# Kernel tuning notes

Measured on AMD Instinct MI355X. Metric: run time of the kernel, lower is better.

Reference implementation:

```python
import jax, jax.numpy as jnp
import numpy as np

B, N = 2048, 16384
K = 256
TEMPERATURE = 1.0


def entmax15(z):
    # alpha=1.5 entmax via exact sort-based threshold (Peters et al. 2019).
    z = z / 2.0
    zs = jnp.flip(jnp.sort(z, axis=-1), axis=-1)          # descending sort [B, N]
    rho = jnp.arange(1, z.shape[-1] + 1, dtype=z.dtype)   # 1..N
    mean = jnp.cumsum(zs, axis=-1) / rho
    mean_sq = jnp.cumsum(zs * zs, axis=-1) / rho
    ss = rho * (mean_sq - mean * mean)
    delta = jnp.clip((1.0 - ss) / rho, 0.0)
    tau = mean - jnp.sqrt(delta)                           # candidate thresholds
    support = jnp.sum(tau <= zs, axis=-1, keepdims=True)   # support size per row
    tau_star = jnp.take_along_axis(tau, support - 1, axis=-1)
    p = jnp.clip(z - tau_star, 0.0) ** 2
    return p


def setup_inputs() -> dict:
    key = jax.random.key(0)
    logits = jax.random.normal(key, (B, N), dtype=jnp.float32)
    return {"logits": logits}


def reference(logits):
    weights = entmax15(logits / TEMPERATURE)
    # top-k mask + renormalize
    _, topk_idx = jax.lax.top_k(weights, K)                # [B, K]
    mask = jnp.zeros_like(weights).at[
        jnp.arange(weights.shape[0])[:, None], topk_idx
    ].set(1.0)
    weights = weights * mask
    weights = weights / (jnp.sum(weights, axis=-1, keepdims=True) + 1e-8)
    num_selected = jnp.sum(weights > 1e-6, axis=-1)
    return weights, num_selected
```

## Files before the change

### kernel.cpp

```cpp
#include <hip/hip_runtime.h>
#include <math.h>

#define BROWS 2048
#define NCOLS 16384
#define NT    1024
#define V4PT  (NCOLS / NT / 4)
#define CAP   512

__global__ __launch_bounds__(NT, 8)
void entmax_fused(const float* __restrict__ in, float* __restrict__ outw,
                  float* __restrict__ outn)
{
    __shared__ float red[4][16];
    __shared__ float redm[16];
    __shared__ float cand[CAP + 4];
    __shared__ float s_zm, s_T, s_tau, s_S;
    __shared__ int   s_cnt, s_nsel;

    const int row  = blockIdx.x;
    const int tid  = threadIdx.x;
    const int lane = tid & 63;
    const int wid  = tid >> 6;
    const float4* rp4 = (const float4*)(in + (size_t)row * NCOLS);
    float4*       wp4 = (float4*)(outw + (size_t)row * NCOLS);

    if (tid == 0) { s_cnt = 0; s_nsel = 0; }

    float4 zr[V4PT];
    float m = -INFINITY;
    #pragma unroll
    for (int it = 0; it < V4PT; ++it) {
        float4 v = rp4[it * NT + tid];
        v.x *= 0.5f; v.y *= 0.5f; v.z *= 0.5f; v.w *= 0.5f;
        zr[it] = v;
        m = fmaxf(m, fmaxf(fmaxf(v.x, v.y), fmaxf(v.z, v.w)));
    }
    #pragma unroll
    for (int off = 1; off < 64; off <<= 1) m = fmaxf(m, __shfl_xor(m, off));
    if (lane == 0) redm[wid] = m;
    __syncthreads();
    if (tid < 64) {
        float v = (lane < 16) ? redm[lane] : -INFINITY;
        #pragma unroll
        for (int off = 1; off < 16; off <<= 1) v = fmaxf(v, __shfl_xor(v, off));
        if (lane == 0) s_zm = v;
    }
    __syncthreads();
    const float zm = s_zm;

    float g0 = 0.f, g1 = 0.f, g2 = 0.f, g3 = 0.f;
    #pragma unroll
    for (int it = 0; it < V4PT; ++it) {
        float4 v = zr[it];
        #pragma unroll
        for (int e = 0; e < 4; ++e) {
            float z = (e == 0) ? v.x : (e == 1) ? v.y : (e == 2) ? v.z : v.w;
            float d3 = z - (zm - 1.0f);
            if (d3 > 0.f) {
                g3 = fmaf(d3, d3, g3);
                float d2 = d3 - 0.25f; if (d2 > 0.f) g2 = fmaf(d2, d2, g2);
                float d1 = d3 - 0.50f; if (d1 > 0.f) g1 = fmaf(d1, d1, g1);
                float d0 = d3 - 0.75f; if (d0 > 0.f) g0 = fmaf(d0, d0, g0);
            }
        }
    }
    #pragma unroll
    for (int off = 1; off < 64; off <<= 1) {
        g0 += __shfl_xor(g0, off); g1 += __shfl_xor(g1, off);
        g2 += __shfl_xor(g2, off); g3 += __shfl_xor(g3, off);
    }
    if (lane == 0) { red[0][wid] = g0; red[1][wid] = g1; red[2][wid] = g2; red[3][wid] = g3; }
    __syncthreads();
    if (tid < 64) {
        int j = lane >> 4, idx = lane & 15;
        float v = red[j][idx];
        #pragma unroll
        for (int off = 1; off < 16; off <<= 1) v += __shfl_xor(v, off);
        float G0 = __shfl(v, 0), G1 = __shfl(v, 16), G2 = __shfl(v, 32), G3 = __shfl(v, 48);
        (void)G3;
        if (lane == 0) {
            float T = zm - 1.0f;
            if      (G0 >= 1.02f) T = zm - 0.25f;
            else if (G1 >= 1.02f) T = zm - 0.50f;
            else if (G2 >= 1.02f) T = zm - 0.75f;
            s_T = T;
        }
    }
    __syncthreads();
    const float T = s_T;

    #pragma unroll
    for (int it = 0; it < V4PT; ++it) {
        float4 v = zr[it];
        if (v.x > T) { int p = atomicAdd(&s_cnt, 1); if (p < CAP) cand[p] = v.x; }
        if (v.y > T) { int p = atomicAdd(&s_cnt, 1); if (p < CAP) cand[p] = v.y; }
        if (v.z > T) { int p = atomicAdd(&s_cnt, 1); if (p < CAP) cand[p] = v.z; }
        if (v.w > T) { int p = atomicAdd(&s_cnt, 1); if (p < CAP) cand[p] = v.w; }
    }
    __syncthreads();

    if (tid < 64) {
        const int C = min(s_cnt, CAP);
        if (lane < 4) cand[C + lane] = -INFINITY;
        const int C4 = (C + 3) >> 2;
        const float4* c4 = (const float4*)cand;
        float lo = T, hi = zm;
        for (int round = 0; round < 3; ++round) {
            float h = (hi - lo) * 0.015625f;
            float t = fmaf(h, (float)(lane + 1), lo);
            float g = 0.f;
            for (int i = 0; i < C4; ++i) {
                float4 v = c4[i]; float d;
                d = v.x - t; if (d > 0.f) g = fmaf(d, d, g);
                d = v.y - t; if (d > 0.f) g = fmaf(d, d, g);
                d = v.z - t; if (d > 0.f) g = fmaf(d, d, g);
                d = v.w - t; if (d > 0.f) g = fmaf(d, d, g);
            }
            unsigned long long bal = __ballot(g >= 1.f);
            float lo_old = lo;
            if (bal == 0ull) hi = lo_old + h;
            else {
                int j = 63 - (int)__clzll((long long)bal);
                lo = fmaf(h, (float)(j + 1), lo_old);
                hi = fmaf(h, (float)(j + 2), lo_old);
            }
        }
        float tau = lo;
        for (int r = 0; r < 3; ++r) {
            float k = 0.f, s1 = 0.f, s2 = 0.f;
            for (int i = 0; i < C4; ++i) {
                float4 v = c4[i];
                if (v.x > tau) { k += 1.f; s1 += v.x; s2 = fmaf(v.x, v.x, s2); }
                if (v.y > tau) { k += 1.f; s1 += v.y; s2 = fmaf(v.y, v.y, s2); }
                if (v.z > tau) { k += 1.f; s1 += v.z; s2 = fmaf(v.z, v.z, s2); }
                if (v.w > tau) { k += 1.f; s1 += v.w; s2 = fmaf(v.w, v.w, s2); }
            }
            if (k < 0.5f) break;
            float mean  = s1 / k;
            float ss    = s2 - mean * s1;
            float delta = fmaxf((1.f - ss) / k, 0.f);
            tau = mean - sqrtf(delta);
        }
        float ps = 0.f;
        for (int i = 0; i < C4; ++i) {
            float4 v = c4[i]; float d;
            d = v.x - tau; if (d > 0.f) ps = fmaf(d, d, ps);
            d = v.y - tau; if (d > 0.f) ps = fmaf(d, d, ps);
            d = v.z - tau; if (d > 0.f) ps = fmaf(d, d, ps);
            d = v.w - tau; if (d > 0.f) ps = fmaf(d, d, ps);
        }
        if (lane == 0) { s_tau = tau; s_S = ps; }
    }
    __syncthreads();
    const float tau_star = s_tau;
    const float rnorm    = 1.0f / (s_S + 1e-8f);

    int lc = 0;
    #pragma unroll
    for (int it = 0; it < V4PT; ++it) {
        float4 v = zr[it];
        float4 w; float d;
        d = fmaxf(v.x - tau_star, 0.f); w.x = d * d * rnorm; lc += (w.x > 1e-6f);
        d = fmaxf(v.y - tau_star, 0.f); w.y = d * d * rnorm; lc += (w.y > 1e-6f);
        d = fmaxf(v.z - tau_star, 0.f); w.z = d * d * rnorm; lc += (w.z > 1e-6f);
        d = fmaxf(v.w - tau_star, 0.f); w.w = d * d * rnorm; lc += (w.w > 1e-6f);
        wp4[it * NT + tid] = w;
    }
    #pragma unroll
    for (int off = 32; off; off >>= 1) lc += __shfl_down(lc, off);
    if (lane == 0) atomicAdd(&s_nsel, lc);
    __syncthreads();
    if (tid == 0) outn[row] = (float)s_nsel;
}

extern "C" void kernel_launch(void* const* d_in, const int* in_sizes, int n_in,
                              void* d_out, int out_size, void* d_ws, size_t ws_size,
                              hipStream_t stream) {
    const float* logits = (const float*)d_in[0];
    float* outw = (float*)d_out;
    float* outn = outw + (size_t)BROWS * NCOLS;
    entmax_fused<<<dim3(BROWS), dim3(NT), 0, stream>>>(logits, outw, outn);
}
```

Measured before the change: 254.0 us.

## Shrink blocks to 256 threads and re-read row from global instead of registers

Switches from a 1024-thread block that holds the whole row in registers to a 256-thread block that streams the row from global memory three times (max, histogram, output), relying on cache for the re-reads. Candidate collection moves into the histogram pass with a larger shared buffer, and a second compaction over that buffer replaces the separate full-row filter pass. Cross-wave reductions become simple serial sums over 4 waves. The aim is lower register pressure and higher occupancy, at the cost of extra global/L2 traffic and more shared-memory atomics on the wider candidate window.

New measurement: 264.6 us. 4.2% more time.

```diff
diff --git a/kernel.cpp b/kernel.cpp
--- a/kernel.cpp
+++ b/kernel.cpp
@@ -3,19 +3,21 @@
 
 #define BROWS 2048
 #define NCOLS 16384
-#define NT    1024
-#define V4PT  (NCOLS / NT / 4)
-#define CAP   512
+#define NT    256
+#define F4T   (NCOLS / NT / 4)
+#define LCAP  3072
+#define CCAP  512
 
 __global__ __launch_bounds__(NT, 8)
 void entmax_fused(const float* __restrict__ in, float* __restrict__ outw,
                   float* __restrict__ outn)
 {
-    __shared__ float red[4][16];
-    __shared__ float redm[16];
-    __shared__ float cand[CAP + 4];
+    __shared__ float cand[LCAP];
+    __shared__ float cand2[CCAP + 4];
+    __shared__ float red[4][4];
+    __shared__ float redm[4];
     __shared__ float s_zm, s_T, s_tau, s_S;
-    __shared__ int   s_cnt, s_nsel;
+    __shared__ int   s_cnt, s_cnt2, s_nsel;
 
     const int row  = blockIdx.x;
     const int tid  = threadIdx.x;
@@ -24,40 +26,35 @@
     const float4* rp4 = (const float4*)(in + (size_t)row * NCOLS);
     float4*       wp4 = (float4*)(outw + (size_t)row * NCOLS);
 
-    if (tid == 0) { s_cnt = 0; s_nsel = 0; }
+    if (tid == 0) { s_cnt = 0; s_cnt2 = 0; s_nsel = 0; }
 
-    float4 zr[V4PT];
     float m = -INFINITY;
-    #pragma unroll
-    for (int it = 0; it < V4PT; ++it) {
+    #pragma unroll 8
+    for (int it = 0; it < F4T; ++it) {
         float4 v = rp4[it * NT + tid];
-        v.x *= 0.5f; v.y *= 0.5f; v.z *= 0.5f; v.w *= 0.5f;
-        zr[it] = v;
         m = fmaxf(m, fmaxf(fmaxf(v.x, v.y), fmaxf(v.z, v.w)));
     }
     #pragma unroll
     for (int off = 1; off < 64; off <<= 1) m = fmaxf(m, __shfl_xor(m, off));
     if (lane == 0) redm[wid] = m;
     __syncthreads();
-    if (tid < 64) {
-        float v = (lane < 16) ? redm[lane] : -INFINITY;
-        #pragma unroll
-        for (int off = 1; off < 16; off <<= 1) v = fmaxf(v, __shfl_xor(v, off));
-        if (lane == 0) s_zm = v;
-    }
+    if (tid == 0)
+        s_zm = 0.5f * fmaxf(fmaxf(redm[0], redm[1]), fmaxf(redm[2], redm[3]));
     __syncthreads();
     const float zm = s_zm;
+    const float TL = zm - 1.0f;
 
     float g0 = 0.f, g1 = 0.f, g2 = 0.f, g3 = 0.f;
-    #pragma unroll
-    for (int it = 0; it < V4PT; ++it) {
-        float4 v = zr[it];
+    #pragma unroll 4
+    for (int it = 0; it < F4T; ++it) {
+        float4 v = rp4[it * NT + tid];
         #pragma unroll
         for (int e = 0; e < 4; ++e) {
-            float z = (e == 0) ? v.x : (e == 1) ? v.y : (e == 2) ? v.z : v.w;
-            float d3 = z - (zm - 1.0f);
+            float z  = 0.5f * ((e == 0) ? v.x : (e == 1) ? v.y : (e == 2) ? v.z : v.w);
+            float d3 = z - TL;
             if (d3 > 0.f) {
                 g3 = fmaf(d3, d3, g3);
+                int p = atomicAdd(&s_cnt, 1); if (p < LCAP) cand[p] = z;
                 float d2 = d3 - 0.25f; if (d2 > 0.f) g2 = fmaf(d2, d2, g2);
                 float d1 = d3 - 0.50f; if (d1 > 0.f) g1 = fmaf(d1, d1, g1);
                 float d0 = d3 - 0.75f; if (d0 > 0.f) g0 = fmaf(d0, d0, g0);
@@ -71,39 +68,33 @@
     }
     if (lane == 0) { red[0][wid] = g0; red[1][wid] = g1; red[2][wid] = g2; red[3][wid] = g3; }
     __syncthreads();
-    if (tid < 64) {
-        int j = lane >> 4, idx = lane & 15;
-        float v = red[j][idx];
-        #pragma unroll
-        for (int off = 1; off < 16; off <<= 1) v += __shfl_xor(v, off);
-        float G0 = __shfl(v, 0), G1 = __shfl(v, 16), G2 = __shfl(v, 32), G3 = __shfl(v, 48);
-        (void)G3;
-        if (lane == 0) {
-            float T = zm - 1.0f;
-            if      (G0 >= 1.02f) T = zm - 0.25f;
-            else if (G1 >= 1.02f) T = zm - 0.50f;
-            else if (G2 >= 1.02f) T = zm - 0.75f;
-            s_T = T;
-        }
+    if (tid == 0) {
+        float G0 = red[0][0] + red[0][1] + red[0][2] + red[0][3];
+        float G1 = red[1][0] + red[1][1] + red[1][2] + red[1][3];
+        float G2 = red[2][0] + red[2][1] + red[2][2] + red[2][3];
+        float T = TL;
+        if      (G0 >= 1.02f) T = zm - 0.25f;
+        else if (G1 >= 1.02f) T = zm - 0.50f;
+        else if (G2 >= 1.02f) T = zm - 0.75f;
+        s_T = T;
     }
     __syncthreads();
     const float T = s_T;
 
-    #pragma unroll
-    for (int it = 0; it < V4PT; ++it) {
-        float4 v = zr[it];
-        if (v.x > T) { int p = atomicAdd(&s_cnt, 1); if (p < CAP) cand[p] = v.x; }
-        if (v.y > T) { int p = atomicAdd(&s_cnt, 1); if (p < CAP) cand[p] = v.y; }
-        if (v.z > T) { int p = atomicAdd(&s_cnt, 1); if (p < CAP) cand[p] = v.z; }
-        if (v.w > T) { int p = atomicAdd(&s_cnt, 1); if (p < CAP) cand[p] = v.w; }
+    {
+        const int C = min(s_cnt, LCAP);
+        for (int i = tid; i < C; i += NT) {
+            float z = cand[i];
+            if (z > T) { int p = atomicAdd(&s_cnt2, 1); if (p < CCAP) cand2[p] = z; }
+        }
     }
     __syncthreads();
 
     if (tid < 64) {
-        const int C = min(s_cnt, CAP);
-        if (lane < 4) cand[C + lane] = -INFINITY;
+        const int C = min(s_cnt2, CCAP);
+        if (lane < 4) cand2[C + lane] = -INFINITY;
         const int C4 = (C + 3) >> 2;
-        const float4* c4 = (const float4*)cand;
+        const float4* c4 = (const float4*)cand2;
         float lo = T, hi = zm;
         for (int round = 0; round < 3; ++round) {
             float h = (hi - lo) * 0.015625f;
@@ -156,14 +147,14 @@
     const float rnorm    = 1.0f / (s_S + 1e-8f);
 
     int lc = 0;
-    #pragma unroll
-    for (int it = 0; it < V4PT; ++it) {
-        float4 v = zr[it];
+    #pragma unroll 8
+    for (int it = 0; it < F4T; ++it) {
+        float4 v = rp4[it * NT + tid];
         float4 w; float d;
-        d = fmaxf(v.x - tau_star, 0.f); w.x = d * d * rnorm; lc += (w.x > 1e-6f);
-        d = fmaxf(v.y - tau_star, 0.f); w.y = d * d * rnorm; lc += (w.y > 1e-6f);
-        d = fmaxf(v.z - tau_star, 0.f); w.z = d * d * rnorm; lc += (w.z > 1e-6f);
-        d = fmaxf(v.w - tau_star, 0.f); w.w = d * d * rnorm; lc += (w.w > 1e-6f);
+        d = fmaxf(0.5f * v.x - tau_star, 0.f); w.x = d * d * rnorm; lc += (w.x > 1e-6f);
+        d = fmaxf(0.5f * v.y - tau_star, 0.f); w.y = d * d * rnorm; lc += (w.y > 1e-6f);
+        d = fmaxf(0.5f * v.z - tau_star, 0.f); w.z = d * d * rnorm; lc += (w.z > 1e-6f);
+        d = fmaxf(0.5f * v.w - tau_star, 0.f); w.w = d * d * rnorm; lc += (w.w > 1e-6f);
         wp4[it * NT + tid] = w;
     }
     #pragma unroll
```

## Process two rows per block with wave-aggregated candidate compaction and nontemporal stores

Applied to the files above, without the earlier changes.

Each 1024-thread block now handles two rows at once. The two rows' reductions and threshold searches run interleaved, and two wavefronts work through the candidate lists in parallel, which is meant to hide the serial single-wave tail phase and the barrier latency. Candidate compaction now uses a ballot, popcount and one atomic per wave instead of a shared atomic per element, and the candidate cap is raised. Output stores use nontemporal hints. In exchange, register pressure doubles (32 float4 per thread), which risks spills or lower occupancy, and there are half as many blocks.

After: 266.6 us. 1.05x slower.

```diff
diff --git a/kernel.cpp b/kernel.cpp
--- a/kernel.cpp
+++ b/kernel.cpp
@@ -4,103 +4,176 @@
 #define BROWS 2048
 #define NCOLS 16384
 #define NT    1024
-#define V4PT  (NCOLS / NT / 4)
-#define CAP   512
+#define F4R   (NCOLS / NT / 4)
+#define CCAP  1024
+
+typedef float f32x4 __attribute__((ext_vector_type(4)));
 
 __global__ __launch_bounds__(NT, 8)
-void entmax_fused(const float* __restrict__ in, float* __restrict__ outw,
-                  float* __restrict__ outn)
+void entmax2(const float* __restrict__ in, float* __restrict__ outw,
+             float* __restrict__ outn)
 {
-    __shared__ float red[4][16];
-    __shared__ float redm[16];
-    __shared__ float cand[CAP + 4];
-    __shared__ float s_zm, s_T, s_tau, s_S;
-    __shared__ int   s_cnt, s_nsel;
-
-    const int row  = blockIdx.x;
+    __shared__ float candA[CCAP + 4], candB[CCAP + 4];
+    __shared__ float redA[4][16], redB[4][16];
+    __shared__ float redmA[16], redmB[16];
+    __shared__ float s_zmA, s_zmB, s_TA, s_TB, s_tauA, s_SA, s_tauB, s_SB;
+    __shared__ int   s_cntA, s_cntB, s_nselA, s_nselB;
+
+    const int pair = blockIdx.x;
+    const int rowA = pair * 2, rowB = pair * 2 + 1;
     const int tid  = threadIdx.x;
     const int lane = tid & 63;
     const int wid  = tid >> 6;
-    const float4* rp4 = (const float4*)(in + (size_t)row * NCOLS);
-    float4*       wp4 = (float4*)(outw + (size_t)row * NCOLS);
-
-    if (tid == 0) { s_cnt = 0; s_nsel = 0; }
-
-    float4 zr[V4PT];
-    float m = -INFINITY;
-    #pragma unroll
-    for (int it = 0; it < V4PT; ++it) {
-        float4 v = rp4[it * NT + tid];
-        v.x *= 0.5f; v.y *= 0.5f; v.z *= 0.5f; v.w *= 0.5f;
-        zr[it] = v;
-        m = fmaxf(m, fmaxf(fmaxf(v.x, v.y), fmaxf(v.z, v.w)));
-    }
-    #pragma unroll
-    for (int off = 1; off < 64; off <<= 1) m = fmaxf(m, __shfl_xor(m, off));
-    if (lane == 0) redm[wid] = m;
-    __syncthreads();
-    if (tid < 64) {
-        float v = (lane < 16) ? redm[lane] : -INFINITY;
+    const float4* rpA = (const float4*)(in + (size_t)rowA * NCOLS);
+    const float4* rpB = (const float4*)(in + (size_t)rowB * NCOLS);
+    f32x4*        wpA = (f32x4*)(outw + (size_t)rowA * NCOLS);
+    f32x4*        wpB = (f32x4*)(outw + (size_t)rowB * NCOLS);
+
+    if (tid == 0) { s_cntA = 0; s_cntB = 0; s_nselA = 0; s_nselB = 0; }
+
+    float4 zrA[F4R], zrB[F4R];
+    #pragma unroll
+    for (int it = 0; it < F4R; ++it) zrA[it] = rpA[it * NT + tid];
+    #pragma unroll
+    for (int it = 0; it < F4R; ++it) zrB[it] = rpB[it * NT + tid];
+    float mA = -INFINITY, mB = -INFINITY;
+    #pragma unroll
+    for (int it = 0; it < F4R; ++it) {
+        float4 a = zrA[it];
+        a.x *= 0.5f; a.y *= 0.5f; a.z *= 0.5f; a.w *= 0.5f; zrA[it] = a;
+        mA = fmaxf(mA, fmaxf(fmaxf(a.x, a.y), fmaxf(a.z, a.w)));
+        float4 b = zrB[it];
+        b.x *= 0.5f; b.y *= 0.5f; b.z *= 0.5f; b.w *= 0.5f; zrB[it] = b;
+        mB = fmaxf(mB, fmaxf(fmaxf(b.x, b.y), fmaxf(b.z, b.w)));
+    }
+    #pragma unroll
+    for (int off = 1; off < 64; off <<= 1) {
+        mA = fmaxf(mA, __shfl_xor(mA, off));
+        mB = fmaxf(mB, __shfl_xor(mB, off));
+    }
+    if (lane == 0) { redmA[wid] = mA; redmB[wid] = mB; }
+    __syncthreads();
+    if (wid == 0) {
+        float v = (lane < 16) ? redmA[lane] : -INFINITY;
         #pragma unroll
         for (int off = 1; off < 16; off <<= 1) v = fmaxf(v, __shfl_xor(v, off));
-        if (lane == 0) s_zm = v;
-    }
-    __syncthreads();
-    const float zm = s_zm;
-
-    float g0 = 0.f, g1 = 0.f, g2 = 0.f, g3 = 0.f;
-    #pragma unroll
-    for (int it = 0; it < V4PT; ++it) {
-        float4 v = zr[it];
+        if (lane == 0) s_zmA = v;
+    } else if (wid == 1) {
+        float v = (lane < 16) ? redmB[lane] : -INFINITY;
+        #pragma unroll
+        for (int off = 1; off < 16; off <<= 1) v = fmaxf(v, __shfl_xor(v, off));
+        if (lane == 0) s_zmB = v;
+    }
+    __syncthreads();
+    const float zmA = s_zmA, zmB = s_zmB;
+    const float TLA = zmA - 1.0f, TLB = zmB - 1.0f;
+
+    float a0 = 0.f, a1 = 0.f, a2 = 0.f, a3 = 0.f;
+    float b0 = 0.f, b1 = 0.f, b2 = 0.f, b3 = 0.f;
+    #pragma unroll
+    for (int it = 0; it < F4R; ++it) {
+        float4 va = zrA[it], vb = zrB[it];
         #pragma unroll
         for (int e = 0; e < 4; ++e) {
-            float z = (e == 0) ? v.x : (e == 1) ? v.y : (e == 2) ? v.z : v.w;
-            float d3 = z - (zm - 1.0f);
+            float za = (e == 0) ? va.x : (e == 1) ? va.y : (e == 2) ? va.z : va.w;
+            float d3 = za - TLA;
             if (d3 > 0.f) {
-                g3 = fmaf(d3, d3, g3);
-                float d2 = d3 - 0.25f; if (d2 > 0.f) g2 = fmaf(d2, d2, g2);
-                float d1 = d3 - 0.50f; if (d1 > 0.f) g1 = fmaf(d1, d1, g1);
-                float d0 = d3 - 0.75f; if (d0 > 0.f) g0 = fmaf(d0, d0, g0);
+                a3 = fmaf(d3, d3, a3);
+                float d2 = d3 - 0.25f; if (d2 > 0.f) a2 = fmaf(d2, d2, a2);
+                float d1 = d3 - 0.50f; if (d1 > 0.f) a1 = fmaf(d1, d1, a1);
+                float d0 = d3 - 0.75f; if (d0 > 0.f) a0 = fmaf(d0, d0, a0);
+            }
+            float zb = (e == 0) ? vb.x : (e == 1) ? vb.y : (e == 2) ? vb.z : vb.w;
+            float e3 = zb - TLB;
+            if (e3 > 0.f) {
+                b3 = fmaf(e3, e3, b3);
+                float e2 = e3 - 0.25f; if (e2 > 0.f) b2 = fmaf(e2, e2, b2);
+                float e1 = e3 - 0.50f; if (e1 > 0.f) b1 = fmaf(e1, e1, b1);
+                float e0 = e3 - 0.75f; if (e0 > 0.f) b0 = fmaf(e0, e0, b0);
             }
         }
     }
     #pragma unroll
     for (int off = 1; off < 64; off <<= 1) {
-        g0 += __shfl_xor(g0, off); g1 += __shfl_xor(g1, off);
-        g2 += __shfl_xor(g2, off); g3 += __shfl_xor(g3, off);
-    }
-    if (lane == 0) { red[0][wid] = g0; red[1][wid] = g1; red[2][wid] = g2; red[3][wid] = g3; }
-    __syncthreads();
-    if (tid < 64) {
+        a0 += __shfl_xor(a0, off); a1 += __shfl_xor(a1, off);
+        a2 += __shfl_xor(a2, off); a3 += __shfl_xor(a3, off);
+        b0 += __shfl_xor(b0, off); b1 += __shfl_xor(b1, off);
+        b2 += __shfl_xor(b2, off); b3 += __shfl_xor(b3, off);
+    }
+    if (lane == 0) {
+        redA[0][wid] = a0; redA[1][wid] = a1; redA[2][wid] = a2; redA[3][wid] = a3;
+        redB[0][wid] = b0; redB[1][wid] = b1; redB[2][wid] = b2; redB[3][wid] = b3;
+    }
+    __syncthreads();
+    if (wid == 0) {
         int j = lane >> 4, idx = lane & 15;
-        float v = red[j][idx];
+        float v = redA[j][idx];
         #pragma unroll
         for (int off = 1; off < 16; off <<= 1) v += __shfl_xor(v, off);
-        float G0 = __shfl(v, 0), G1 = __shfl(v, 16), G2 = __shfl(v, 32), G3 = __shfl(v, 48);
-        (void)G3;
+        float G0 = __shfl(v, 0), G1 = __shfl(v, 16), G2 = __shfl(v, 32);
         if (lane == 0) {
-            float T = zm - 1.0f;
-            if      (G0 >= 1.02f) T = zm - 0.25f;
-            else if (G1 >= 1.02f) T = zm - 0.50f;
-            else if (G2 >= 1.02f) T = zm - 0.75f;
-            s_T = T;
-        }
-    }
-    __syncthreads();
-    const float T = s_T;
-
-    #pragma unroll
-    for (int it = 0; it < V4PT; ++it) {
-        float4 v = zr[it];
-        if (v.x > T) { int p = atomicAdd(&s_cnt, 1); if (p < CAP) cand[p] = v.x; }
-        if (v.y > T) { int p = atomicAdd(&s_cnt, 1); if (p < CAP) cand[p] = v.y; }
-        if (v.z > T) { int p = atomicAdd(&s_cnt, 1); if (p < CAP) cand[p] = v.z; }
-        if (v.w > T) { int p = atomicAdd(&s_cnt, 1); if (p < CAP) cand[p] = v.w; }
-    }
-    __syncthreads();
-
-    if (tid < 64) {
-        const int C = min(s_cnt, CAP);
+            float T = TLA;
+            if      (G0 >= 1.02f) T = zmA - 0.25f;
+            else if (G1 >= 1.02f) T = zmA - 0.50f;
+            else if (G2 >= 1.02f) T = zmA - 0.75f;
+            s_TA = T;
+        }
+    } else if (wid == 1) {
+        int j = lane >> 4, idx = lane & 15;
+        float v = redB[j][idx];
+        #pragma unroll
+        for (int off = 1; off < 16; off <<= 1) v += __shfl_xor(v, off);
+        float G0 = __shfl(v, 0), G1 = __shfl(v, 16), G2 = __shfl(v, 32);
+        if (lane == 0) {
+            float T = TLB;
+            if      (G0 >= 1.02f) T = zmB - 0.25f;
+            else if (G1 >= 1.02f) T = zmB - 0.50f;
+            else if (G2 >= 1.02f) T = zmB - 0.75f;
+            s_TB = T;
+        }
+    }
+    __syncthreads();
+    const float TA = s_TA, TB = s_TB;
+
+    const unsigned long long ltmask = (1ull << lane) - 1ull;
+    #pragma unroll
+    for (int it = 0; it < F4R; ++it) {
+        float4 va = zrA[it], vb = zrB[it];
+        #pragma unroll
+        for (int e = 0; e < 4; ++e) {
+            float za = (e == 0) ? va.x : (e == 1) ? va.y : (e == 2) ? va.z : va.w;
+            bool pa = (za > TA);
+            unsigned long long ma = __ballot(pa);
+            if (ma) {
+                int base = 0;
+                if (lane == 0) base = atomicAdd(&s_cntA, (int)__popcll(ma));
+                base = __shfl(base, 0);
+                if (pa) {
+                    int p = base + (int)__popcll(ma & ltmask);
+                    if (p < CCAP) candA[p] = za;
+                }
+            }
+            float zb = (e == 0) ? vb.x : (e == 1) ? vb.y : (e == 2) ? vb.z : vb.w;
+            bool pb = (zb > TB);
+            unsigned long long mb = __ballot(pb);
+            if (mb) {
+                int base = 0;
+                if (lane == 0) base = atomicAdd(&s_cntB, (int)__popcll(mb));
+                base = __shfl(base, 0);
+                if (pb) {
+                    int p = base + (int)__popcll(mb & ltmask);
+                    if (p < CCAP) candB[p] = zb;
+                }
+            }
+        }
+    }
+    __syncthreads();
+
+    if (wid < 2) {
+        float* cand = (wid == 0) ? candA : candB;
+        const int   C  = min((wid == 0) ? s_cntA : s_cntB, CCAP);
+        const float T  = (wid == 0) ? TA : TB;
+        const float zm = (wid == 0) ? zmA : zmB;
         if (lane < 4) cand[C + lane] = -INFINITY;
         const int C4 = (C + 3) >> 2;
         const float4* c4 = (const float4*)cand;
@@ -149,28 +222,43 @@
             d = v.z - tau; if (d > 0.f) ps = fmaf(d, d, ps);
             d = v.w - tau; if (d > 0.f) ps = fmaf(d, d, ps);
         }
-        if (lane == 0) { s_tau = tau; s_S = ps; }
-    }
-    __syncthreads();
-    const float tau_star = s_tau;
-    const float rnorm    = 1.0f / (s_S + 1e-8f);
-
-    int lc = 0;
-    #pragma unroll
-    for (int it = 0; it < V4PT; ++it) {
-        float4 v = zr[it];
-        float4 w; float d;
-        d = fmaxf(v.x - tau_star, 0.f); w.x = d * d * rnorm; lc += (w.x > 1e-6f);
-        d = fmaxf(v.y - tau_star, 0.f); w.y = d * d * rnorm; lc += (w.y > 1e-6f);
-        d = fmaxf(v.z - tau_star, 0.f); w.z = d * d * rnorm; lc += (w.z > 1e-6f);
-        d = fmaxf(v.w - tau_star, 0.f); w.w = d * d * rnorm; lc += (w.w > 1e-6f);
-        wp4[it * NT + tid] = w;
-    }
-    #pragma unroll
-    for (int off = 32; off; off >>= 1) lc += __shfl_down(lc, off);
-    if (lane == 0) atomicAdd(&s_nsel, lc);
-    __syncthreads();
-    if (tid == 0) outn[row] = (float)s_nsel;
+        if (lane == 0) {
+            if (wid == 0) { s_tauA = tau; s_SA = ps; }
+            else          { s_tauB = tau; s_SB = ps; }
+        }
+    }
+    __syncthreads();
+    const float tauA = s_tauA, rnA = 1.0f / (s_SA + 1e-8f);
+    const float tauB = s_tauB, rnB = 1.0f / (s_SB + 1e-8f);
+
+    int lcA = 0, lcB = 0;
+    #pragma unroll
+    for (int it = 0; it < F4R; ++it) {
+        float4 va = zrA[it];
+        f32x4 w; float d;
+        d = fmaxf(va.x - tauA, 0.f); w.x = d * d * rnA; lcA += (w.x > 1e-6f);
+        d = fmaxf(va.y - tauA, 0.f); w.y = d * d * rnA; lcA += (w.y > 1e-6f);
+        d = fmaxf(va.z - tauA, 0.f); w.z = d * d * rnA; lcA += (w.z > 1e-6f);
+        d = fmaxf(va.w - tauA, 0.f); w.w = d * d * rnA; lcA += (w.w > 1e-6f);
+        __builtin_nontemporal_store(w, &wpA[it * NT + tid]);
+        float4 vb = zrB[it];
+        d = fmaxf(vb.x - tauB, 0.f); w.x = d * d * rnB; lcB += (w.x > 1e-6f);
+        d = fmaxf(vb.y - tauB, 0.f); w.y = d * d * rnB; lcB += (w.y > 1e-6f);
+        d = fmaxf(vb.z - tauB, 0.f); w.z = d * d * rnB; lcB += (w.z > 1e-6f);
+        d = fmaxf(vb.w - tauB, 0.f); w.w = d * d * rnB; lcB += (w.w > 1e-6f);
+        __builtin_nontemporal_store(w, &wpB[it * NT + tid]);
+    }
+    #pragma unroll
+    for (int off = 32; off; off >>= 1) {
+        lcA += __shfl_down(lcA, off);
+        lcB += __shfl_down(lcB, off);
+    }
+    if (lane == 0) { atomicAdd(&s_nselA, lcA); atomicAdd(&s_nselB, lcB); }
+    __syncthreads();
+    if (tid == 0) {
+        outn[rowA] = (float)s_nselA;
+        outn[rowB] = (float)s_nselB;
+    }
 }
 
 extern "C" void kernel_launch(void* const* d_in, const int* in_sizes, int n_in,
@@ -179,5 +267,5 @@
     const float* logits = (const float*)d_in[0];
     float* outw = (float*)d_out;
     float* outn = outw + (size_t)BROWS * NCOLS;
-    entmax_fused<<<dim3(BROWS), dim3(NT), 0, stream>>>(logits, outw, outn);
+    entmax2<<<dim3(BROWS / 2), dim3(NT), 0, stream>>>(logits, outw, outn);
 }
```
